# Performance work log

Hardware: AMD Instinct MI355X
Metric: run time of the kernel (lower is better)

The kernel has to match this reference:

```python
import jax, jax.numpy as jnp
import numpy as np

E, B, F, L = 4, 8192, 2048, 100  # envs, batch/env, feature dim, num classes
LAM = 1.0  # hparams['RERM_lam']


def setup_inputs() -> dict:
    key = jax.random.key(0)
    k1, k2, k3 = jax.random.split(key, 3)
    feats = jax.random.normal(k1, (E, B, F), jnp.float32)
    y = jax.random.randint(k2, (E, B), 0, L)
    W = jax.random.normal(k3, (F, L), jnp.float32) * 0.02
    b = jnp.zeros((L,), jnp.float32)
    return {"feats": feats, "y": y, "W": W, "b": b}


def _rerm_loss(feats, y, W, b):
    # --- per-(label, env) masked means (mean_table / visit_table) ---
    onehot = jax.nn.one_hot(y, L, dtype=feats.dtype)          # [E,B,L]
    counts = onehot.sum(axis=1)                               # [E,L]
    sums = jnp.einsum('ebl,ebf->elf', onehot, feats)          # [E,L,F]
    means = sums / jnp.maximum(counts, 1.0)[..., None]        # [E,L,F]
    visit = (counts > 0).astype(feats.dtype)                  # [E,L]

    # --- torch.var(mean_table[i, fetch_envs, :], dim=1): variance over
    # feature dim per env (unbiased, /(F-1)), then mean over visited envs ---
    mu = means.mean(axis=-1, keepdims=True)                   # [E,L,1]
    var = jnp.sum((means - mu) ** 2, axis=-1) / (F - 1)       # [E,L]

    nvis = visit.sum(axis=0)                                  # [L]
    sel = (nvis > 1.5).astype(feats.dtype)                    # labels with >1 env
    per_label = (var * visit).sum(axis=0) / jnp.maximum(nvis, 1.0)  # [L]
    nzlabel = jnp.maximum(sel.sum(), 1.0)
    mean_loss = LAM * jnp.sum(per_label * sel) / nzlabel

    # --- cross-entropy over all envs concatenated ---
    logits = feats.reshape(E * B, F) @ W + b                  # [E*B,L]
    logp = jax.nn.log_softmax(logits, axis=-1)
    ce = -jnp.take_along_axis(logp, y.reshape(-1, 1), axis=1).mean()

    return mean_loss + ce


def reference(feats, y, W, b):
    return _rerm_loss(feats, y, W, b)
```

## Files before the change

### kernel.cpp

```cpp
#include <hip/hip_runtime.h>
#include <hip/hip_bf16.h>
#include <math.h>

#define E 4
#define B 8192
#define F 2048
#define L 100
#define NROWS (E * B)
#define LAMBDA 1.0f

typedef __attribute__((ext_vector_type(8))) short bf16x8;
typedef __attribute__((ext_vector_type(4))) float f32x4;

static __device__ inline unsigned short f2bf(float x) {
    unsigned u = __float_as_uint(x);
    unsigned r = (u + 0x7FFFu + ((u >> 16) & 1u)) >> 16;
    return (unsigned short)r;
}

#define SG 4
#define NSG 25
#define SBS 8
#define SRW (B / SBS)
#define NSUM (E * SBS * NSG)

#define GBM 128
#define NGEMM (NROWS / GBM)

__global__ void __launch_bounds__(256) k_prep(const float* __restrict__ W,
                                              unsigned short* __restrict__ Wt,
                                              float* __restrict__ ce_accum,
                                              int* __restrict__ counts) {
    __shared__ float st[64][101];
    int t = threadIdx.x;
    int b = blockIdx.x;
    if (b == 0) {
        for (int i = t; i < E * L; i += 256) counts[i] = 0;
        if (t == 0) ce_accum[0] = 0.f;
    }
    int k0 = b * 64;
    for (int i = t; i < 64 * 100; i += 256) {
        st[i / 100][i % 100] = W[(size_t)k0 * L + i];
    }
    __syncthreads();
    for (int i = t; i < 112 * 32; i += 256) {
        int n = i >> 5, kp = i & 31;
        unsigned lo = 0, hi = 0;
        if (n < L) {
            lo = f2bf(st[kp * 2][n]);
            hi = f2bf(st[kp * 2 + 1][n]);
        }
        *(unsigned*)&Wt[(size_t)n * F + k0 + kp * 2] = lo | (hi << 16);
    }
}

static __device__ inline unsigned pack_bf(float lo, float hi) {
    unsigned ul = __float_as_uint(lo) + 0x8000u;
    unsigned uh = __float_as_uint(hi) + 0x8000u;
    return __builtin_amdgcn_perm(uh, ul, 0x07060302u);
}

__global__ void __launch_bounds__(512, 4) k_main(const float* __restrict__ feats,
                                                 const int* __restrict__ y,
                                                 const unsigned short* __restrict__ Wt,
                                                 const float* __restrict__ bias,
                                                 float* __restrict__ partial,
                                                 int* __restrict__ counts,
                                                 float* __restrict__ ce_accum) {
    __shared__ __align__(16) char sm[6208];
    int t = threadIdx.x;

    if (blockIdx.x < NGEMM) {
        float* red = (float*)sm;
        int wave = t >> 6, lane = t & 63;
        int quad = lane >> 4, l16 = lane & 15;
        int row = blockIdx.x * GBM + wave * 16 + l16;
        const float* ap = feats + (size_t)row * F + quad * 8;
        const unsigned short* wbase = Wt + (size_t)l16 * F + quad * 8;

        f32x4 acc[7];
#pragma unroll
        for (int ct = 0; ct < 7; ++ct) acc[ct] = (f32x4){0.f, 0.f, 0.f, 0.f};

        float4 na0 = ((const float4*)ap)[0];
        float4 na1 = ((const float4*)ap)[1];
#pragma unroll 2
        for (int kk = 0; kk < F / 32; ++kk) {
            float4 a0 = na0, a1 = na1;
            if (kk + 1 < F / 32) {
                const float* apn = ap + (size_t)(kk + 1) * 32;
                na0 = ((const float4*)apn)[0];
                na1 = ((const float4*)apn)[1];
            }
            union { unsigned w[4]; bf16x8 v; } bb;
            bb.w[0] = pack_bf(a0.x, a0.y);
            bb.w[1] = pack_bf(a0.z, a0.w);
            bb.w[2] = pack_bf(a1.x, a1.y);
            bb.w[3] = pack_bf(a1.z, a1.w);
#pragma unroll
            for (int ct = 0; ct < 7; ++ct) {
                bf16x8 af = *(const bf16x8*)(wbase + (size_t)ct * 16 * F + kk * 32);
                acc[ct] = __builtin_amdgcn_mfma_f32_16x16x32_bf16(af, bb.v, acc[ct], 0, 0, 0);
            }
        }

        int lab = y[row];
        float vv[7][4];
        float vm = -1e30f;
#pragma unroll
        for (int ct = 0; ct < 7; ++ct) {
#pragma unroll
            for (int r = 0; r < 4; ++r) {
                int c = ct * 16 + quad * 4 + r;
                float bb2 = (c < L) ? bias[c] : 0.f;
                float v = acc[ct][r] + bb2;
                vv[ct][r] = v;
                if (c < L) vm = fmaxf(vm, v);
            }
        }
        vm = fmaxf(vm, __shfl_xor(vm, 16));
        vm = fmaxf(vm, __shfl_xor(vm, 32));
        float se = 0.f, tv = 0.f;
#pragma unroll
        for (int ct = 0; ct < 7; ++ct) {
#pragma unroll
            for (int r = 0; r < 4; ++r) {
                int c = ct * 16 + quad * 4 + r;
                if (c < L) se += __expf(vv[ct][r] - vm);
                if (c == lab) tv = vv[ct][r];
            }
        }
        se += __shfl_xor(se, 16);
        se += __shfl_xor(se, 32);
        tv += __shfl_xor(tv, 16);
        tv += __shfl_xor(tv, 32);
        float ce = vm + __logf(se) - tv;
#pragma unroll
        for (int s = 1; s <= 8; s <<= 1) ce += __shfl_xor(ce, s);
        if (lane == 0) red[wave] = ce;
        __syncthreads();
        if (t == 0) {
            float v = 0.f;
#pragma unroll
            for (int w = 0; w < 8; ++w) v += red[w];
            atomicAdd(ce_accum, v);
        }
    } else {
        int* ys = (int*)sm;
        unsigned short* list = (unsigned short*)(sm + 4096);
        int* cnt4 = (int*)(sm + 4096 + 2048);
        int* ntot = (int*)(sm + 4096 + 2048 + 16);
        int bi = blockIdx.x - NGEMM;
        int lg = bi % NSG;
        int bs = (bi / NSG) % SBS;
        int e  = bi / (NSG * SBS);
        int lab0 = lg * SG;

        if (t < SG) cnt4[t] = 0;
        if (t == 8) ntot[0] = 0;
        const int* yb = y + e * B + bs * SRW;
        ys[t] = yb[t];
        ys[t + 512] = yb[t + 512];
        __syncthreads();

        for (int r = t; r < SRW; r += 512) {
            int lb = ys[r] - lab0;
            if ((unsigned)lb < SG) {
                atomicAdd(&cnt4[lb], 1);
                int p = atomicAdd(ntot, 1);
                list[p] = (unsigned short)(r | (lb << 10));
            }
        }
        __syncthreads();
        int n = ntot[0];
        int npad = (n + 3) & ~3;
        if (t < npad - n) list[n + t] = 0;
        __syncthreads();

        const float* fb = feats + ((size_t)e * B + (size_t)bs * SRW) * F + t * 4;
        float4 a0 = make_float4(0.f, 0.f, 0.f, 0.f);
        float4 a1 = a0, a2 = a0, a3 = a0;

        float4 x[4];
        int tg[4];
        if (n > 0) {
#pragma unroll
            for (int j = 0; j < 4; ++j) {
                int ev = list[j];
                tg[j] = ev >> 10;
                x[j] = *(const float4*)(fb + (size_t)(ev & 1023) * F);
            }
            for (int i = 0; i < npad; i += 4) {
                float4 nx[4];
                int ntg[4];
                if (i + 4 < npad) {
#pragma unroll
                    for (int j = 0; j < 4; ++j) {
                        int ev = list[i + 4 + j];
                        ntg[j] = ev >> 10;
                        nx[j] = *(const float4*)(fb + (size_t)(ev & 1023) * F);
                    }
                }
#pragma unroll
                for (int j = 0; j < 4; ++j) {
                    if (i + j < n) {
                        float4 v = x[j];
                        int g = tg[j];
                        if (g == 0)      { a0.x += v.x; a0.y += v.y; a0.z += v.z; a0.w += v.w; }
                        else if (g == 1) { a1.x += v.x; a1.y += v.y; a1.z += v.z; a1.w += v.w; }
                        else if (g == 2) { a2.x += v.x; a2.y += v.y; a2.z += v.z; a2.w += v.w; }
                        else             { a3.x += v.x; a3.y += v.y; a3.z += v.z; a3.w += v.w; }
                    }
                }
#pragma unroll
                for (int j = 0; j < 4; ++j) { x[j] = nx[j]; tg[j] = ntg[j]; }
            }
        }

        float* pb = partial + (((size_t)e * SBS + bs) * L + lab0) * F + t * 4;
        *(float4*)(pb + 0 * F) = a0;
        *(float4*)(pb + 1 * F) = a1;
        *(float4*)(pb + 2 * F) = a2;
        *(float4*)(pb + 3 * F) = a3;
        if (t < SG) atomicAdd(&counts[e * L + lab0 + t], cnt4[t]);
    }
}

__global__ void __launch_bounds__(512) k_var(const float* __restrict__ partial,
                                             const int* __restrict__ counts,
                                             float* __restrict__ var_out) {
    int el = blockIdx.x;
    int e = el / L, l = el % L;
    int t = threadIdx.x;
    float inv = 1.f / fmaxf((float)counts[el], 1.f);
    float4 s = make_float4(0.f, 0.f, 0.f, 0.f);
#pragma unroll
    for (int bs = 0; bs < SBS; ++bs) {
        float4 v = *(const float4*)&partial[(((size_t)e * SBS + bs) * L + l) * F + t * 4];
        s.x += v.x; s.y += v.y; s.z += v.z; s.w += v.w;
    }
    float mx = s.x * inv, my = s.y * inv, mz = s.z * inv, mw = s.w * inv;
    float sm = mx + my + mz + mw;
    float sm2 = mx * mx + my * my + mz * mz + mw * mw;
#pragma unroll
    for (int sft = 1; sft <= 32; sft <<= 1) {
        sm += __shfl_xor(sm, sft);
        sm2 += __shfl_xor(sm2, sft);
    }
    __shared__ float r1[8], r2[8];
    int wv = t >> 6, ln = t & 63;
    if (ln == 0) { r1[wv] = sm; r2[wv] = sm2; }
    __syncthreads();
    if (t == 0) {
        float S = 0.f, S2 = 0.f;
#pragma unroll
        for (int w = 0; w < 8; ++w) { S += r1[w]; S2 += r2[w]; }
        var_out[el] = (S2 - S * S / (float)F) / (float)(F - 1);
    }
}

__global__ void k_final(const int* __restrict__ counts,
                        const float* __restrict__ var_in,
                        const float* __restrict__ ce_accum,
                        float* __restrict__ out) {
    __shared__ float s_sum[128], s_cnt[128];
    int t = threadIdx.x;
    float selsum = 0.f, selcnt = 0.f;
    for (int l = t; l < L; l += 128) {
        float nvis = 0.f, vsum = 0.f;
        for (int e = 0; e < E; ++e) {
            if (counts[e * L + l] > 0) { nvis += 1.f; vsum += var_in[e * L + l]; }
        }
        float per_label = vsum / fmaxf(nvis, 1.f);
        if (nvis > 1.5f) { selsum += per_label; selcnt += 1.f; }
    }
    s_sum[t] = selsum; s_cnt[t] = selcnt;
    __syncthreads();
    for (int s = 64; s > 0; s >>= 1) {
        if (t < s) { s_sum[t] += s_sum[t + s]; s_cnt[t] += s_cnt[t + s]; }
        __syncthreads();
    }
    if (t == 0) {
        float mean_loss = LAMBDA * s_sum[0] / fmaxf(s_cnt[0], 1.f);
        float ce = ce_accum[0] / (float)NROWS;
        out[0] = mean_loss + ce;
    }
}

extern "C" void kernel_launch(void* const* d_in, const int* in_sizes, int n_in,
                              void* d_out, int out_size, void* d_ws, size_t ws_size,
                              hipStream_t stream) {
    const float* feats = (const float*)d_in[0];
    const int*   y     = (const int*)d_in[1];
    const float* Wm    = (const float*)d_in[2];
    const float* bias  = (const float*)d_in[3];
    float* out = (float*)d_out;

    char* ws = (char*)d_ws;
    float*          ce_accum = (float*)ws;
    int*            counts   = (int*)(ws + 256);
    float*          var_buf  = (float*)(ws + 2048);
    float*          partial  = (float*)(ws + 4096);
    unsigned short* Wt       = (unsigned short*)(ws + 4096 + (size_t)E * SBS * L * F * 4);

    k_prep<<<F / 64, 256, 0, stream>>>(Wm, Wt, ce_accum, counts);
    k_main<<<NGEMM + NSUM, 512, 0, stream>>>(feats, y, Wt, bias, partial, counts, ce_accum);
    k_var<<<E * L, 512, 0, stream>>>(partial, counts, var_buf);
    k_final<<<1, 128, 0, stream>>>(counts, var_buf, ce_accum, out);
}
```

Before: 491.6 us.

## Deepen GEMM prefetch pipeline and shrink fused kernel blocks to 256 threads

The GEMM branch now keeps four K-steps of activation loads and two K-steps of W fragments in flight in registers, replacing the one-step lookahead. The block size drops from 512 to 256 threads with half the rows per block, and the launch bounds change to (256,3). The segment-sum branch has each thread cover 8 features with two float4 loads so the same 2048-wide rows are handled by fewer threads. The aim is to hide global-memory latency better and raise memory-level parallelism, at the cost of more registers per thread and possibly lower occupancy.

After: 525.0 us. 6.8% more time.

```diff
diff --git a/kernel.cpp b/kernel.cpp
--- a/kernel.cpp
+++ b/kernel.cpp
@@ -24,8 +24,9 @@
 #define SRW (B / SBS)
 #define NSUM (E * SBS * NSG)
 
-#define GBM 128
+#define GBM 64
 #define NGEMM (NROWS / GBM)
+#define NK (F / 32)
 
 __global__ void __launch_bounds__(256) k_prep(const float* __restrict__ W,
                                               unsigned short* __restrict__ Wt,
@@ -60,7 +61,7 @@
     return __builtin_amdgcn_perm(uh, ul, 0x07060302u);
 }
 
-__global__ void __launch_bounds__(512, 4) k_main(const float* __restrict__ feats,
+__global__ void __launch_bounds__(256, 3) k_main(const float* __restrict__ feats,
                                                  const int* __restrict__ y,
                                                  const unsigned short* __restrict__ Wt,
                                                  const float* __restrict__ bias,
@@ -82,25 +83,38 @@
 #pragma unroll
         for (int ct = 0; ct < 7; ++ct) acc[ct] = (f32x4){0.f, 0.f, 0.f, 0.f};
 
-        float4 na0 = ((const float4*)ap)[0];
-        float4 na1 = ((const float4*)ap)[1];
-#pragma unroll 2
-        for (int kk = 0; kk < F / 32; ++kk) {
-            float4 a0 = na0, a1 = na1;
-            if (kk + 1 < F / 32) {
-                const float* apn = ap + (size_t)(kk + 1) * 32;
-                na0 = ((const float4*)apn)[0];
-                na1 = ((const float4*)apn)[1];
-            }
-            union { unsigned w[4]; bf16x8 v; } bb;
-            bb.w[0] = pack_bf(a0.x, a0.y);
-            bb.w[1] = pack_bf(a0.z, a0.w);
-            bb.w[2] = pack_bf(a1.x, a1.y);
-            bb.w[3] = pack_bf(a1.z, a1.w);
-#pragma unroll
-            for (int ct = 0; ct < 7; ++ct) {
-                bf16x8 af = *(const bf16x8*)(wbase + (size_t)ct * 16 * F + kk * 32);
-                acc[ct] = __builtin_amdgcn_mfma_f32_16x16x32_bf16(af, bb.v, acc[ct], 0, 0, 0);
+        float4 pa[4][2];
+        bf16x8 pw[2][7];
+#pragma unroll
+        for (int j = 0; j < 4; ++j) {
+            pa[j][0] = ((const float4*)(ap + j * 32))[0];
+            pa[j][1] = ((const float4*)(ap + j * 32))[1];
+        }
+#pragma unroll
+        for (int cw = 0; cw < 2; ++cw)
+#pragma unroll
+            for (int ct = 0; ct < 7; ++ct)
+                pw[cw][ct] = *(const bf16x8*)(wbase + (size_t)ct * 16 * F + cw * 32);
+
+        for (int k4 = 0; k4 < NK; k4 += 4) {
+#pragma unroll
+            for (int s = 0; s < 4; ++s) {
+                int kk = k4 + s;
+                union { unsigned w[4]; bf16x8 v; } bb;
+                bb.w[0] = pack_bf(pa[s][0].x, pa[s][0].y);
+                bb.w[1] = pack_bf(pa[s][0].z, pa[s][0].w);
+                bb.w[2] = pack_bf(pa[s][1].x, pa[s][1].y);
+                bb.w[3] = pack_bf(pa[s][1].z, pa[s][1].w);
+                int ka = (kk + 4 < NK) ? kk + 4 : NK - 1;
+                pa[s][0] = ((const float4*)(ap + ka * 32))[0];
+                pa[s][1] = ((const float4*)(ap + ka * 32))[1];
+#pragma unroll
+                for (int ct = 0; ct < 7; ++ct)
+                    acc[ct] = __builtin_amdgcn_mfma_f32_16x16x32_bf16(pw[s & 1][ct], bb.v, acc[ct], 0, 0, 0);
+                int kw = (kk + 2 < NK) ? kk + 2 : NK - 1;
+#pragma unroll
+                for (int ct = 0; ct < 7; ++ct)
+                    pw[s & 1][ct] = *(const bf16x8*)(wbase + (size_t)ct * 16 * F + kw * 32);
             }
         }
 
@@ -140,9 +154,7 @@
         if (lane == 0) red[wave] = ce;
         __syncthreads();
         if (t == 0) {
-            float v = 0.f;
-#pragma unroll
-            for (int w = 0; w < 8; ++w) v += red[w];
+            float v = red[0] + red[1] + red[2] + red[3];
             atomicAdd(ce_accum, v);
         }
     } else {
@@ -159,11 +171,11 @@
         if (t < SG) cnt4[t] = 0;
         if (t == 8) ntot[0] = 0;
         const int* yb = y + e * B + bs * SRW;
-        ys[t] = yb[t];
-        ys[t + 512] = yb[t + 512];
-        __syncthreads();
-
-        for (int r = t; r < SRW; r += 512) {
+#pragma unroll
+        for (int j = 0; j < 4; ++j) ys[t + j * 256] = yb[t + j * 256];
+        __syncthreads();
+
+        for (int r = t; r < SRW; r += 256) {
             int lb = ys[r] - lab0;
             if ((unsigned)lb < SG) {
                 atomicAdd(&cnt4[lb], 1);
@@ -177,51 +189,70 @@
         if (t < npad - n) list[n + t] = 0;
         __syncthreads();
 
-        const float* fb = feats + ((size_t)e * B + (size_t)bs * SRW) * F + t * 4;
-        float4 a0 = make_float4(0.f, 0.f, 0.f, 0.f);
-        float4 a1 = a0, a2 = a0, a3 = a0;
-
-        float4 x[4];
+        const float* fb = feats + ((size_t)e * B + (size_t)bs * SRW) * F + t * 8;
+        float4 a0l = make_float4(0.f, 0.f, 0.f, 0.f), a0h = a0l;
+        float4 a1l = a0l, a1h = a0l, a2l = a0l, a2h = a0l, a3l = a0l, a3h = a0l;
+
+        float4 x[4][2];
         int tg[4];
         if (n > 0) {
 #pragma unroll
             for (int j = 0; j < 4; ++j) {
                 int ev = list[j];
                 tg[j] = ev >> 10;
-                x[j] = *(const float4*)(fb + (size_t)(ev & 1023) * F);
+                const float* p = fb + (size_t)(ev & 1023) * F;
+                x[j][0] = ((const float4*)p)[0];
+                x[j][1] = ((const float4*)p)[1];
             }
             for (int i = 0; i < npad; i += 4) {
-                float4 nx[4];
+                float4 nx[4][2];
                 int ntg[4];
                 if (i + 4 < npad) {
 #pragma unroll
                     for (int j = 0; j < 4; ++j) {
                         int ev = list[i + 4 + j];
                         ntg[j] = ev >> 10;
-                        nx[j] = *(const float4*)(fb + (size_t)(ev & 1023) * F);
+                        const float* p = fb + (size_t)(ev & 1023) * F;
+                        nx[j][0] = ((const float4*)p)[0];
+                        nx[j][1] = ((const float4*)p)[1];
                     }
                 }
 #pragma unroll
                 for (int j = 0; j < 4; ++j) {
                     if (i + j < n) {
-                        float4 v = x[j];
+                        float4 vl = x[j][0], vh = x[j][1];
                         int g = tg[j];
-                        if (g == 0)      { a0.x += v.x; a0.y += v.y; a0.z += v.z; a0.w += v.w; }
-                        else if (g == 1) { a1.x += v.x; a1.y += v.y; a1.z += v.z; a1.w += v.w; }
-                        else if (g == 2) { a2.x += v.x; a2.y += v.y; a2.z += v.z; a2.w += v.w; }
-                        else             { a3.x += v.x; a3.y += v.y; a3.z += v.z; a3.w += v.w; }
+                        if (g == 0) {
+                            a0l.x += vl.x; a0l.y += vl.y; a0l.z += vl.z; a0l.w += vl.w;
+                            a0h.x += vh.x; a0h.y += vh.y; a0h.z += vh.z; a0h.w += vh.w;
+                        } else if (g == 1) {
+                            a1l.x += vl.x; a1l.y += vl.y; a1l.z += vl.z; a1l.w += vl.w;
+                            a1h.x += vh.x; a1h.y += vh.y; a1h.z += vh.z; a1h.w += vh.w;
+                        } else if (g == 2) {
+                            a2l.x += vl.x; a2l.y += vl.y; a2l.z += vl.z; a2l.w += vl.w;
+                            a2h.x += vh.x; a2h.y += vh.y; a2h.z += vh.z; a2h.w += vh.w;
+                        } else {
+                            a3l.x += vl.x; a3l.y += vl.y; a3l.z += vl.z; a3l.w += vl.w;
+                            a3h.x += vh.x; a3h.y += vh.y; a3h.z += vh.z; a3h.w += vh.w;
+                        }
                     }
                 }
 #pragma unroll
-                for (int j = 0; j < 4; ++j) { x[j] = nx[j]; tg[j] = ntg[j]; }
-            }
-        }
-
-        float* pb = partial + (((size_t)e * SBS + bs) * L + lab0) * F + t * 4;
-        *(float4*)(pb + 0 * F) = a0;
-        *(float4*)(pb + 1 * F) = a1;
-        *(float4*)(pb + 2 * F) = a2;
-        *(float4*)(pb + 3 * F) = a3;
+                for (int j = 0; j < 4; ++j) {
+                    x[j][0] = nx[j][0]; x[j][1] = nx[j][1]; tg[j] = ntg[j];
+                }
+            }
+        }
+
+        float* pb = partial + (((size_t)e * SBS + bs) * L + lab0) * F + t * 8;
+        ((float4*)(pb + 0 * F))[0] = a0l;
+        ((float4*)(pb + 0 * F))[1] = a0h;
+        ((float4*)(pb + 1 * F))[0] = a1l;
+        ((float4*)(pb + 1 * F))[1] = a1h;
+        ((float4*)(pb + 2 * F))[0] = a2l;
+        ((float4*)(pb + 2 * F))[1] = a2h;
+        ((float4*)(pb + 3 * F))[0] = a3l;
+        ((float4*)(pb + 3 * F))[1] = a3h;
         if (t < SG) atomicAdd(&counts[e * L + lab0 + t], cnt4[t]);
     }
 }
@@ -304,7 +335,7 @@
     unsigned short* Wt       = (unsigned short*)(ws + 4096 + (size_t)E * SBS * L * F * 4);
 
     k_prep<<<F / 64, 256, 0, stream>>>(Wm, Wt, ce_accum, counts);
-    k_main<<<NGEMM + NSUM, 512, 0, stream>>>(feats, y, Wt, bias, partial, counts, ce_accum);
+    k_main<<<NGEMM + NSUM, 256, 0, stream>>>(feats, y, Wt, bias, partial, counts, ce_accum);
     k_var<<<E * L, 512, 0, stream>>>(partial, counts, var_buf);
     k_final<<<1, 128, 0, stream>>>(counts, var_buf, ce_accum, out);
 }
```

## Stage GEMM tiles in LDS, split classes across waves, interleave GEMM and sum blocks

Applied to the files above, without the earlier changes.

The GEMM path now uses 32-row blocks that stage bf16 A and W tiles (64-wide K chunks) in shared memory. Each of the four wave pairs computes a subset of the class tiles, and softmax max, sum and target values are combined across waves through LDS. Block indices are interleaved so that 9 of every 16 blocks do GEMM and 7 do the masked label sums. This is meant to balance the two workloads across the GPU, replace direct global W reads with shared-memory reuse, and raise occupancy (launch bounds 512,8). In exchange it adds more barriers and a larger shared-memory footprint per block.

New measurement: 413.2 us. 1.19x faster.

```diff
diff --git a/kernel.cpp b/kernel.cpp
--- a/kernel.cpp
+++ b/kernel.cpp
@@ -24,8 +24,12 @@
 #define SRW (B / SBS)
 #define NSUM (E * SBS * NSG)
 
-#define GBM 128
+#define GBM 32
+#define GKC 64
+#define APAD 72
 #define NGEMM (NROWS / GBM)
+#define NBASE 115
+#define NBLK (NBASE * 16)
 
 __global__ void __launch_bounds__(256) k_prep(const float* __restrict__ W,
                                               unsigned short* __restrict__ Wt,
@@ -60,100 +64,134 @@
     return __builtin_amdgcn_perm(uh, ul, 0x07060302u);
 }
 
-__global__ void __launch_bounds__(512, 4) k_main(const float* __restrict__ feats,
+__global__ void __launch_bounds__(512, 8) k_main(const float* __restrict__ feats,
                                                  const int* __restrict__ y,
                                                  const unsigned short* __restrict__ Wt,
                                                  const float* __restrict__ bias,
                                                  float* __restrict__ partial,
                                                  int* __restrict__ counts,
                                                  float* __restrict__ ce_accum) {
-    __shared__ __align__(16) char sm[6208];
+    __shared__ __align__(16) char sm[22400];
     int t = threadIdx.x;
-
-    if (blockIdx.x < NGEMM) {
-        float* red = (float*)sm;
+    int u = blockIdx.x;
+    int br = u & 15, base = u >> 4;
+
+    if (br < 9) {
+        int gid = base * 9 + br;
+        if (gid >= NGEMM) return;
+        unsigned short* As = (unsigned short*)sm;
+        unsigned short* Ws = As + GBM * APAD;
+        float* pmaxs = (float*)(sm + 20736);
+        float* psums = pmaxs + 128;
+        float* ptgts = psums + 128;
+        float* ceg   = ptgts + 128;
         int wave = t >> 6, lane = t & 63;
         int quad = lane >> 4, l16 = lane & 15;
-        int row = blockIdx.x * GBM + wave * 16 + l16;
-        const float* ap = feats + (size_t)row * F + quad * 8;
-        const unsigned short* wbase = Wt + (size_t)l16 * F + quad * 8;
-
-        f32x4 acc[7];
-#pragma unroll
-        for (int ct = 0; ct < 7; ++ct) acc[ct] = (f32x4){0.f, 0.f, 0.f, 0.f};
-
-        float4 na0 = ((const float4*)ap)[0];
-        float4 na1 = ((const float4*)ap)[1];
-#pragma unroll 2
-        for (int kk = 0; kk < F / 32; ++kk) {
-            float4 a0 = na0, a1 = na1;
-            if (kk + 1 < F / 32) {
-                const float* apn = ap + (size_t)(kk + 1) * 32;
-                na0 = ((const float4*)apn)[0];
-                na1 = ((const float4*)apn)[1];
-            }
-            union { unsigned w[4]; bf16x8 v; } bb;
-            bb.w[0] = pack_bf(a0.x, a0.y);
-            bb.w[1] = pack_bf(a0.z, a0.w);
-            bb.w[2] = pack_bf(a1.x, a1.y);
-            bb.w[3] = pack_bf(a1.z, a1.w);
-#pragma unroll
-            for (int ct = 0; ct < 7; ++ct) {
-                bf16x8 af = *(const bf16x8*)(wbase + (size_t)ct * 16 * F + kk * 32);
-                acc[ct] = __builtin_amdgcn_mfma_f32_16x16x32_bf16(af, bb.v, acc[ct], 0, 0, 0);
-            }
-        }
-
-        int lab = y[row];
-        float vv[7][4];
+        int g = wave >> 2, h = wave & 3;
+        size_t row0 = (size_t)gid * GBM;
+
+        int arow = t >> 4, acol = (t & 15) * 4;
+        const float* aptr = feats + (row0 + arow) * (size_t)F + acol;
+        int w1row = t >> 3, w1c = (t & 7) * 8;
+        int w2row = (512 + t) >> 3, w2c = ((512 + t) & 7) * 8;
+        const unsigned short* wp1 = Wt + (size_t)w1row * F + w1c;
+        const unsigned short* wp2 = (t < 384) ? Wt + (size_t)w2row * F + w2c : Wt;
+
+        f32x4 acc0 = (f32x4){0.f, 0.f, 0.f, 0.f};
+        f32x4 acc1 = acc0;
+
+        float4 pa = *(const float4*)aptr;
+        uint4 pw1 = *(const uint4*)wp1;
+        uint4 pw2 = *(const uint4*)wp2;
+
+        for (int k0 = 0; k0 < F; k0 += GKC) {
+            __syncthreads();
+            unsigned u0 = pack_bf(pa.x, pa.y), u1 = pack_bf(pa.z, pa.w);
+            *(uint2*)&As[arow * APAD + acol] = make_uint2(u0, u1);
+            *(uint4*)&Ws[w1row * APAD + w1c] = pw1;
+            if (t < 384) *(uint4*)&Ws[w2row * APAD + w2c] = pw2;
+            __syncthreads();
+            if (k0 + GKC < F) {
+                pa  = *(const float4*)(aptr + k0 + GKC);
+                pw1 = *(const uint4*)(wp1 + k0 + GKC);
+                pw2 = *(const uint4*)(wp2 + k0 + GKC);
+            }
+#pragma unroll
+            for (int ks = 0; ks < 2; ++ks) {
+                bf16x8 bfr = *(const bf16x8*)&As[(g * 16 + l16) * APAD + ks * 32 + quad * 8];
+                bf16x8 af0 = *(const bf16x8*)&Ws[((2 * h) * 16 + l16) * APAD + ks * 32 + quad * 8];
+                acc0 = __builtin_amdgcn_mfma_f32_16x16x32_bf16(af0, bfr, acc0, 0, 0, 0);
+                if (h < 3) {
+                    bf16x8 af1 = *(const bf16x8*)&Ws[((2 * h + 1) * 16 + l16) * APAD + ks * 32 + quad * 8];
+                    acc1 = __builtin_amdgcn_mfma_f32_16x16x32_bf16(af1, bfr, acc1, 0, 0, 0);
+                }
+            }
+        }
+
+        int rl = g * 16 + l16;
+        int lab = y[row0 + rl];
+        float vv[2][4];
         float vm = -1e30f;
 #pragma unroll
-        for (int ct = 0; ct < 7; ++ct) {
+        for (int j = 0; j < 2; ++j) {
 #pragma unroll
             for (int r = 0; r < 4; ++r) {
+                int ct = 2 * h + j;
                 int c = ct * 16 + quad * 4 + r;
-                float bb2 = (c < L) ? bias[c] : 0.f;
-                float v = acc[ct][r] + bb2;
-                vv[ct][r] = v;
-                if (c < L) vm = fmaxf(vm, v);
+                float v = (j == 0) ? acc0[r] : acc1[r];
+                float bb = (c < L) ? bias[c] : 0.f;
+                v += bb;
+                vv[j][r] = v;
+                bool valid = (c < L) && (j == 0 || h < 3);
+                if (valid) vm = fmaxf(vm, v);
             }
         }
         vm = fmaxf(vm, __shfl_xor(vm, 16));
         vm = fmaxf(vm, __shfl_xor(vm, 32));
+        if (lane < 16) pmaxs[h * 32 + rl] = vm;
+        __syncthreads();
+        float M = fmaxf(fmaxf(pmaxs[rl], pmaxs[32 + rl]),
+                        fmaxf(pmaxs[64 + rl], pmaxs[96 + rl]));
         float se = 0.f, tv = 0.f;
 #pragma unroll
-        for (int ct = 0; ct < 7; ++ct) {
+        for (int j = 0; j < 2; ++j) {
 #pragma unroll
             for (int r = 0; r < 4; ++r) {
+                int ct = 2 * h + j;
                 int c = ct * 16 + quad * 4 + r;
-                if (c < L) se += __expf(vv[ct][r] - vm);
-                if (c == lab) tv = vv[ct][r];
+                bool valid = (c < L) && (j == 0 || h < 3);
+                if (valid) se += __expf(vv[j][r] - M);
+                if (valid && c == lab) tv += vv[j][r];
             }
         }
         se += __shfl_xor(se, 16);
         se += __shfl_xor(se, 32);
         tv += __shfl_xor(tv, 16);
         tv += __shfl_xor(tv, 32);
-        float ce = vm + __logf(se) - tv;
-#pragma unroll
-        for (int s = 1; s <= 8; s <<= 1) ce += __shfl_xor(ce, s);
-        if (lane == 0) red[wave] = ce;
-        __syncthreads();
-        if (t == 0) {
-            float v = 0.f;
-#pragma unroll
-            for (int w = 0; w < 8; ++w) v += red[w];
-            atomicAdd(ce_accum, v);
-        }
+        if (lane < 16) { psums[h * 32 + rl] = se; ptgts[h * 32 + rl] = tv; }
+        __syncthreads();
+        if (h == 0 && lane < 16) {
+            float SE = psums[rl] + psums[32 + rl] + psums[64 + rl] + psums[96 + rl];
+            float TV = ptgts[rl] + ptgts[32 + rl] + ptgts[64 + rl] + ptgts[96 + rl];
+            float ce = M + __logf(SE) - TV;
+            ce += __shfl_xor(ce, 1);
+            ce += __shfl_xor(ce, 2);
+            ce += __shfl_xor(ce, 4);
+            ce += __shfl_xor(ce, 8);
+            if (lane == 0) ceg[g] = ce;
+        }
+        __syncthreads();
+        if (t == 0) atomicAdd(ce_accum, ceg[0] + ceg[1]);
     } else {
+        int sid = base * 7 + (br - 9);
+        if (sid >= NSUM) return;
         int* ys = (int*)sm;
         unsigned short* list = (unsigned short*)(sm + 4096);
         int* cnt4 = (int*)(sm + 4096 + 2048);
         int* ntot = (int*)(sm + 4096 + 2048 + 16);
-        int bi = blockIdx.x - NGEMM;
-        int lg = bi % NSG;
-        int bs = (bi / NSG) % SBS;
-        int e  = bi / (NSG * SBS);
+        int lg = sid % NSG;
+        int bs = (sid / NSG) % SBS;
+        int e  = sid / (NSG * SBS);
         int lab0 = lg * SG;
 
         if (t < SG) cnt4[t] = 0;
@@ -205,11 +243,11 @@
                 for (int j = 0; j < 4; ++j) {
                     if (i + j < n) {
                         float4 v = x[j];
-                        int g = tg[j];
-                        if (g == 0)      { a0.x += v.x; a0.y += v.y; a0.z += v.z; a0.w += v.w; }
-                        else if (g == 1) { a1.x += v.x; a1.y += v.y; a1.z += v.z; a1.w += v.w; }
-                        else if (g == 2) { a2.x += v.x; a2.y += v.y; a2.z += v.z; a2.w += v.w; }
-                        else             { a3.x += v.x; a3.y += v.y; a3.z += v.z; a3.w += v.w; }
+                        int g2 = tg[j];
+                        if (g2 == 0)      { a0.x += v.x; a0.y += v.y; a0.z += v.z; a0.w += v.w; }
+                        else if (g2 == 1) { a1.x += v.x; a1.y += v.y; a1.z += v.z; a1.w += v.w; }
+                        else if (g2 == 2) { a2.x += v.x; a2.y += v.y; a2.z += v.z; a2.w += v.w; }
+                        else              { a3.x += v.x; a3.y += v.y; a3.z += v.z; a3.w += v.w; }
                     }
                 }
 #pragma unroll
@@ -304,7 +342,7 @@
     unsigned short* Wt       = (unsigned short*)(ws + 4096 + (size_t)E * SBS * L * F * 4);
 
     k_prep<<<F / 64, 256, 0, stream>>>(Wm, Wt, ce_accum, counts);
-    k_main<<<NGEMM + NSUM, 512, 0, stream>>>(feats, y, Wt, bias, partial, counts, ce_accum);
+    k_main<<<NBLK, 512, 0, stream>>>(feats, y, Wt, bias, partial, counts, ce_accum);
     k_var<<<E * L, 512, 0, stream>>>(partial, counts, var_buf);
     k_final<<<1, 128, 0, stream>>>(counts, var_buf, ce_accum, out);
 }
```
